# Performance work log

Measured on AMD Instinct MI355X. Metric: run time of the kernel, lower is better.

The kernel has to match this reference:

```python
import jax, jax.numpy as jnp
import numpy as np

N = 100000
E = 1000000
IN_C = 256
HID = 64
OUT = 64
NEG_SLOPE = 0.2


def setup_inputs() -> dict:
    key = jax.random.key(0)
    ks = jax.random.split(key, 12)
    x = jax.random.normal(ks[0], (N, IN_C), dtype=jnp.float32)
    edge_index = jax.random.randint(ks[1], (2, E), 0, N, dtype=jnp.int64)
    s = 1.0 / np.sqrt(IN_C)
    W1 = jax.random.uniform(ks[2], (IN_C, HID), jnp.float32, -s, s)
    a1_src = jax.random.uniform(ks[3], (HID,), jnp.float32, -s, s)
    a1_dst = jax.random.uniform(ks[4], (HID,), jnp.float32, -s, s)
    b1 = jnp.zeros((HID,), jnp.float32)
    s2 = 1.0 / np.sqrt(HID)
    W2 = jax.random.uniform(ks[5], (HID, OUT), jnp.float32, -s2, s2)
    a2_src = jax.random.uniform(ks[6], (OUT,), jnp.float32, -s2, s2)
    a2_dst = jax.random.uniform(ks[7], (OUT,), jnp.float32, -s2, s2)
    b2 = jnp.zeros((OUT,), jnp.float32)
    return {"x": x, "edge_index": edge_index, "W1": W1, "a1_src": a1_src,
            "a1_dst": a1_dst, "b1": b1, "W2": W2, "a2_src": a2_src,
            "a2_dst": a2_dst, "b2": b2}


def gat_conv(x, W, a_src, a_dst, b, src, dst):
    h = x @ W                              # [N, d]
    alpha_s = h @ a_src                    # [N]
    alpha_d = h @ a_dst                    # [N]
    e = jax.nn.leaky_relu(alpha_s[src] + alpha_d[dst], NEG_SLOPE)  # [E]
    # segment softmax over incoming edges of each destination node
    e_max = jax.lax.stop_gradient(jax.ops.segment_max(e, dst, num_segments=N))
    ex = jnp.exp(e - e_max[dst])
    denom = jax.ops.segment_sum(ex, dst, num_segments=N)
    alpha = ex / (denom[dst] + 1e-16)      # [E]
    out = jax.ops.segment_sum(alpha[:, None] * h[src], dst, num_segments=N)
    return out + b


def reference(x, edge_index, W1, a1_src, a1_dst, b1, W2, a2_src, a2_dst, b2):
    src, dst = edge_index[0], edge_index[1]
    # dropout(p=0.6) is identity in eval mode
    h = jax.nn.relu(gat_conv(x, W1, a1_src, a1_dst, b1, src, dst))
    out = gat_conv(h, W2, a2_src, a2_dst, b2, src, dst)
    return out
```

## Files before the change

### kernel.cpp

```cpp
#include <hip/hip_runtime.h>
#include <math.h>

#define HID 64
#define BSH 9
#define NPB 512
#define EPB 4096
#define CAP 8192

typedef __attribute__((ext_vector_type(8))) short bf16x8;
typedef __attribute__((ext_vector_type(4))) float f32x4;
typedef __attribute__((ext_vector_type(4))) unsigned int u32x4;
typedef __attribute__((ext_vector_type(2))) unsigned int u32x2;

__device__ __forceinline__ unsigned short f2bf(float f) {
    unsigned u = __float_as_uint(f);
    unsigned r = u + 0x7FFF + ((u >> 16) & 1);
    return (unsigned short)(r >> 16);
}


__global__ __launch_bounds__(256) void prep_kernel(const float* __restrict__ W1,
                                                   const float* __restrict__ W2,
                                                   unsigned short* __restrict__ Wt1,
                                                   unsigned short* __restrict__ Wt2,
                                                   int* __restrict__ bcnt) {
    int t = threadIdx.x, blk = blockIdx.x;
    int n = t & 63;
    if (blk == 0) bcnt[t] = 0;
    if (blk < 64) {
        int k = blk * 4 + (t >> 6);
        Wt1[(size_t)n * 256 + k] = f2bf(W1[(size_t)k * 64 + n]);
    } else {
        int k = (blk - 64) * 4 + (t >> 6);
        Wt2[(size_t)n * 64 + k] = f2bf(W2[(size_t)k * 64 + n]);
    }
}


__global__ __launch_bounds__(256) void scatter_gemm1(
    const int* __restrict__ esrc, const int* __restrict__ edst,
    int* __restrict__ bcnt, int* __restrict__ ebuf, int E_, int NB, int SB,
    const float* __restrict__ Xf, const unsigned short* __restrict__ Wt,
    const float* __restrict__ a_s, const float* __restrict__ a_d,
    unsigned short* __restrict__ C, float* __restrict__ as_,
    float* __restrict__ ad_, int Nrows) {
    constexpr int K = 256, KPAD = K + 8, XPAD = 72;
    __shared__ union {
        unsigned short gemm[64 * KPAD + 128 * XPAD];
        struct { int hist[256]; int chunk[256]; int lcur[256]; } sc;
    } sh;
    int t = threadIdx.x;

    if ((int)blockIdx.x < SB) {
        sh.sc.hist[t] = 0;
        sh.sc.lcur[t] = 0;
        __syncthreads();
        int base = blockIdx.x * EPB;
        int lim = E_ - base;
        if (lim > EPB) lim = EPB;
        for (int i = t; i < lim; i += 256) {
            atomicAdd(&sh.sc.hist[edst[base + i] >> BSH], 1);
        }
        __syncthreads();
        if (t < NB) sh.sc.chunk[t] = sh.sc.hist[t] ? atomicAdd(&bcnt[t], sh.sc.hist[t]) : 0;
        __syncthreads();
        for (int i = t; i < lim; i += 256) {
            int sv = esrc[base + i];
            int dv = edst[base + i];
            int b = dv >> BSH;
            int pos = sh.sc.chunk[b] + atomicAdd(&sh.sc.lcur[b], 1);
            ebuf[b * CAP + pos] = (sv << BSH) | (dv & (NPB - 1));
        }
        return;
    }

    unsigned short* Ws = sh.gemm;
    unsigned short* Xs = sh.gemm + 64 * KPAD;
    int n0 = ((int)blockIdx.x - SB) * 128;
    int lane = t & 63;
    int w = t >> 6;
    int m = lane & 15;
    int q = lane >> 4;
    int base = n0 + w * 32;

    constexpr int KC8 = K / 8;
    for (int i = t; i < 64 * KC8; i += 256) {
        int n = i / KC8;
        int kc = i % KC8;
        u32x4 v = *(const u32x4*)(Wt + (size_t)n * K + kc * 8);
        *(u32x4*)(&Ws[n * KPAD + kc * 8]) = v;
    }

    f32x4 acc[2][4];
#pragma unroll
    for (int mi = 0; mi < 2; ++mi)
#pragma unroll
        for (int ct = 0; ct < 4; ++ct) acc[mi][ct] = (f32x4){0.f, 0.f, 0.f, 0.f};

    for (int k0 = 0; k0 < K; k0 += 64) {
#pragma unroll
        for (int i = 0; i < 8; ++i) {
            int idx = i * 256 + t;
            int row = idx >> 4;
            int kq = (idx & 15) * 4;
            int gn = n0 + row;
            if (gn >= Nrows) gn = Nrows - 1;
            float4 v = *(const float4*)(Xf + (size_t)gn * K + k0 + kq);
            ushort4 bb;
            bb.x = f2bf(v.x); bb.y = f2bf(v.y); bb.z = f2bf(v.z); bb.w = f2bf(v.w);
            *(ushort4*)(&Xs[row * XPAD + kq]) = bb;
        }
        __syncthreads();
#pragma unroll
        for (int ks = 0; ks < 64; ks += 32) {
            bf16x8 a0 = *(const bf16x8*)(&Xs[(w * 32 + m) * XPAD + ks + q * 8]);
            bf16x8 a1 = *(const bf16x8*)(&Xs[(w * 32 + 16 + m) * XPAD + ks + q * 8]);
#pragma unroll
            for (int ct = 0; ct < 4; ++ct) {
                bf16x8 bv = *(const bf16x8*)(&Ws[(ct * 16 + m) * KPAD + k0 + ks + q * 8]);
                acc[0][ct] = __builtin_amdgcn_mfma_f32_16x16x32_bf16(a0, bv, acc[0][ct], 0, 0, 0);
                acc[1][ct] = __builtin_amdgcn_mfma_f32_16x16x32_bf16(a1, bv, acc[1][ct], 0, 0, 0);
            }
        }
        __syncthreads();
    }

    float sa0 = a_s[m], sa1 = a_s[16 + m], sa2 = a_s[32 + m], sa3 = a_s[48 + m];
    float da0 = a_d[m], da1 = a_d[16 + m], da2 = a_d[32 + m], da3 = a_d[48 + m];

#pragma unroll
    for (int mi = 0; mi < 2; ++mi) {
#pragma unroll
        for (int r = 0; r < 4; ++r) {
            int row = base + mi * 16 + q * 4 + r;
            if (row < Nrows) {
                size_t ro = (size_t)row * 64 + m;
                C[ro]      = f2bf(acc[mi][0][r]);
                C[ro + 16] = f2bf(acc[mi][1][r]);
                C[ro + 32] = f2bf(acc[mi][2][r]);
                C[ro + 48] = f2bf(acc[mi][3][r]);
            }
        }
        float vs[4], vd[4];
#pragma unroll
        for (int r = 0; r < 4; ++r) {
            float s = acc[mi][0][r] * sa0 + acc[mi][1][r] * sa1 +
                      acc[mi][2][r] * sa2 + acc[mi][3][r] * sa3;
            float d = acc[mi][0][r] * da0 + acc[mi][1][r] * da1 +
                      acc[mi][2][r] * da2 + acc[mi][3][r] * da3;
#pragma unroll
            for (int o = 1; o < 16; o <<= 1) {
                s += __shfl_xor(s, o);
                d += __shfl_xor(d, o);
            }
            vs[r] = s;
            vd[r] = d;
        }
        if (m < 4) {
            int row = base + mi * 16 + q * 4 + m;
            float wvs = (m == 0) ? vs[0] : (m == 1) ? vs[1] : (m == 2) ? vs[2] : vs[3];
            float wvd = (m == 0) ? vd[0] : (m == 1) ? vd[1] : (m == 2) ? vd[2] : vd[3];
            if (row < Nrows) {
                as_[row] = wvs;
                ad_[row] = wvd;
            }
        }
    }
}


__global__ __launch_bounds__(256) void csr_build(const int* __restrict__ ebuf,
                                                 const int* __restrict__ bcnt,
                                                 int2* __restrict__ offs,
                                                 int* __restrict__ srcs, int Nv) {
    __shared__ int dhist[NPB], dbase[NPB], psum[256];
    int b = blockIdx.x, t = threadIdx.x;
    int cnt = bcnt[b];
    int e0 = b * CAP;
#pragma unroll
    for (int j = t; j < NPB; j += 256) dhist[j] = 0;
    __syncthreads();
    for (int i = t; i < cnt; i += 256) {
        atomicAdd(&dhist[ebuf[e0 + i] & (NPB - 1)], 1);
    }
    __syncthreads();
    int a0 = dhist[2 * t], a1 = dhist[2 * t + 1];
    psum[t] = a0 + a1;
    __syncthreads();
    for (int o = 1; o < 256; o <<= 1) {
        int u = (t >= o) ? psum[t - o] : 0;
        __syncthreads();
        psum[t] += u;
        __syncthreads();
    }
    int ex = psum[t] - (a0 + a1);
    dbase[2 * t] = ex;
    dbase[2 * t + 1] = ex + a0;
    __syncthreads();
#pragma unroll
    for (int j = t; j < NPB; j += 256) {
        int node = (b << BSH) + j;
        if (node < Nv) {
            int beg = e0 + dbase[j];
            offs[node] = make_int2(beg, beg + dhist[j]);
        }
    }
    __syncthreads();
    for (int i = t; i < cnt; i += 256) {
        int e = ebuf[e0 + i];
        int pos = atomicAdd(&dbase[e & (NPB - 1)], 1);
        srcs[e0 + pos] = e >> BSH;
    }
}


template <int K, bool BF16IN>
__global__ __launch_bounds__(256) void gemm_mfma(const void* __restrict__ Xv,
                                                 const unsigned short* __restrict__ Wt,
                                                 const float* __restrict__ a_s,
                                                 const float* __restrict__ a_d,
                                                 unsigned short* __restrict__ C,
                                                 float* __restrict__ as_,
                                                 float* __restrict__ ad_, int Nrows) {
    constexpr int KPAD = K + 8;
    constexpr int XPAD = 72;
    __shared__ __align__(16) unsigned short Ws[64 * KPAD];
    __shared__ __align__(16) unsigned short Xs[128 * XPAD];

    const float* Xf = (const float*)Xv;
    const unsigned short* Xb = (const unsigned short*)Xv;

    int t = threadIdx.x;
    int n0 = blockIdx.x * 128;
    int lane = t & 63;
    int w = t >> 6;
    int m = lane & 15;
    int q = lane >> 4;
    int base = n0 + w * 32;

    constexpr int KC8 = K / 8;
    for (int i = t; i < 64 * KC8; i += 256) {
        int n = i / KC8;
        int kc = i % KC8;
        u32x4 v = *(const u32x4*)(Wt + (size_t)n * K + kc * 8);
        *(u32x4*)(&Ws[n * KPAD + kc * 8]) = v;
    }

    f32x4 acc[2][4];
#pragma unroll
    for (int mi = 0; mi < 2; ++mi)
#pragma unroll
        for (int ct = 0; ct < 4; ++ct) acc[mi][ct] = (f32x4){0.f, 0.f, 0.f, 0.f};

    for (int k0 = 0; k0 < K; k0 += 64) {
        if (!BF16IN) {
#pragma unroll
            for (int i = 0; i < 8; ++i) {
                int idx = i * 256 + t;
                int row = idx >> 4;
                int kq = (idx & 15) * 4;
                int gn = n0 + row;
                if (gn >= Nrows) gn = Nrows - 1;
                float4 v = *(const float4*)(Xf + (size_t)gn * K + k0 + kq);
                ushort4 bb;
                bb.x = f2bf(v.x); bb.y = f2bf(v.y); bb.z = f2bf(v.z); bb.w = f2bf(v.w);
                *(ushort4*)(&Xs[row * XPAD + kq]) = bb;
            }
        } else {
#pragma unroll
            for (int i = 0; i < 4; ++i) {
                int idx = i * 256 + t;
                int row = idx >> 3;
                int kq = (idx & 7) * 8;
                int gn = n0 + row;
                if (gn >= Nrows) gn = Nrows - 1;
                u32x4 v = *(const u32x4*)(Xb + (size_t)gn * K + k0 + kq);
                *(u32x4*)(&Xs[row * XPAD + kq]) = v;
            }
        }
        __syncthreads();
#pragma unroll
        for (int ks = 0; ks < 64; ks += 32) {
            bf16x8 a0 = *(const bf16x8*)(&Xs[(w * 32 + m) * XPAD + ks + q * 8]);
            bf16x8 a1 = *(const bf16x8*)(&Xs[(w * 32 + 16 + m) * XPAD + ks + q * 8]);
#pragma unroll
            for (int ct = 0; ct < 4; ++ct) {
                bf16x8 bv = *(const bf16x8*)(&Ws[(ct * 16 + m) * KPAD + k0 + ks + q * 8]);
                acc[0][ct] = __builtin_amdgcn_mfma_f32_16x16x32_bf16(a0, bv, acc[0][ct], 0, 0, 0);
                acc[1][ct] = __builtin_amdgcn_mfma_f32_16x16x32_bf16(a1, bv, acc[1][ct], 0, 0, 0);
            }
        }
        __syncthreads();
    }

    float sa0 = a_s[m], sa1 = a_s[16 + m], sa2 = a_s[32 + m], sa3 = a_s[48 + m];
    float da0 = a_d[m], da1 = a_d[16 + m], da2 = a_d[32 + m], da3 = a_d[48 + m];

#pragma unroll
    for (int mi = 0; mi < 2; ++mi) {
#pragma unroll
        for (int r = 0; r < 4; ++r) {
            int row = base + mi * 16 + q * 4 + r;
            if (row < Nrows) {
                size_t ro = (size_t)row * 64 + m;
                C[ro]      = f2bf(acc[mi][0][r]);
                C[ro + 16] = f2bf(acc[mi][1][r]);
                C[ro + 32] = f2bf(acc[mi][2][r]);
                C[ro + 48] = f2bf(acc[mi][3][r]);
            }
        }
        float vs[4], vd[4];
#pragma unroll
        for (int r = 0; r < 4; ++r) {
            float s = acc[mi][0][r] * sa0 + acc[mi][1][r] * sa1 +
                      acc[mi][2][r] * sa2 + acc[mi][3][r] * sa3;
            float d = acc[mi][0][r] * da0 + acc[mi][1][r] * da1 +
                      acc[mi][2][r] * da2 + acc[mi][3][r] * da3;
#pragma unroll
            for (int o = 1; o < 16; o <<= 1) {
                s += __shfl_xor(s, o);
                d += __shfl_xor(d, o);
            }
            vs[r] = s;
            vd[r] = d;
        }
        if (m < 4) {
            int row = base + mi * 16 + q * 4 + m;
            float wvs = (m == 0) ? vs[0] : (m == 1) ? vs[1] : (m == 2) ? vs[2] : vs[3];
            float wvd = (m == 0) ? vd[0] : (m == 1) ? vd[1] : (m == 2) ? vd[2] : vd[3];
            if (row < Nrows) {
                as_[row] = wvs;
                ad_[row] = wvd;
            }
        }
    }
}


#define GATHER_CHUNK(sC, pC, BASE_E)                                          \
    {                                                                         \
        int rem = cnt - (BASE_E);                                             \
        if (rem > 0) {                                                        \
            int nb = rem < 16 ? ((rem + 7) & ~7) : 16;                        \
            for (int j = 0; j < nb; j += 8) {                                 \
                u32x2 hv[8];                                                  \
                float pv[8];                                                  \
                _Pragma("unroll") for (int u = 0; u < 8; ++u) {               \
                    int idx = qsel | (j + u);                                 \
                    int su = __shfl(sC, idx);                                 \
                    pv[u] = __shfl(pC, idx);                                  \
                    hv[u] = *(const u32x2*)(Hp + (size_t)su * HID);           \
                }                                                             \
                _Pragma("unroll") for (int u = 0; u < 8; ++u) {               \
                    acc0 += pv[u] * __uint_as_float(hv[u].x << 16);           \
                    acc1 += pv[u] * __uint_as_float(hv[u].x & 0xFFFF0000u);   \
                    acc2 += pv[u] * __uint_as_float(hv[u].y << 16);           \
                    acc3 += pv[u] * __uint_as_float(hv[u].y & 0xFFFF0000u);   \
                }                                                             \
            }                                                                 \
        }                                                                     \
    }

template <bool RELU_BF16OUT>
__global__ __launch_bounds__(256) void agg_kernel(const unsigned short* __restrict__ H,
                                                  const float* __restrict__ as_,
                                                  const float* __restrict__ ad_,
                                                  const float* __restrict__ bias,
                                                  const int2* __restrict__ offs,
                                                  const int* __restrict__ srcs,
                                                  void* __restrict__ outp, int Nrows) {
    int t = threadIdx.x;
    int lane = t & 63;
    int q16 = lane & 15;
    int qsel = lane & 48;
    int d = blockIdx.x * 16 + ((t >> 6) << 2) + (qsel >> 4);
    if (d >= Nrows) return;
    int2 oe = offs[d];
    int begin = oe.x;
    int cnt = oe.y - oe.x;
    if (cnt > 64) cnt = 64;
    float adv = ad_[d];

    int s0 = 0, s1 = 0, s2 = 0, s3 = 0;
    float p0 = 0.f, p1 = 0.f, p2 = 0.f, p3 = 0.f;
    if (q16 < cnt) {
        s0 = srcs[begin + q16];
        float xv = as_[s0] + adv;
        xv = (xv > 0.f) ? xv : 0.2f * xv;
        p0 = __expf(xv);
    }
    if (16 + q16 < cnt) {
        s1 = srcs[begin + 16 + q16];
        float xv = as_[s1] + adv;
        xv = (xv > 0.f) ? xv : 0.2f * xv;
        p1 = __expf(xv);
    }
    if (32 + q16 < cnt) {
        s2 = srcs[begin + 32 + q16];
        float xv = as_[s2] + adv;
        xv = (xv > 0.f) ? xv : 0.2f * xv;
        p2 = __expf(xv);
    }
    if (48 + q16 < cnt) {
        s3 = srcs[begin + 48 + q16];
        float xv = as_[s3] + adv;
        xv = (xv > 0.f) ? xv : 0.2f * xv;
        p3 = __expf(xv);
    }
    float lsum = (p0 + p1) + (p2 + p3);
#pragma unroll
    for (int o = 1; o < 16; o <<= 1) lsum += __shfl_xor(lsum, o);

    float acc0 = 0.f, acc1 = 0.f, acc2 = 0.f, acc3 = 0.f;
    const unsigned short* Hp = H + 4 * q16;
    GATHER_CHUNK(s0, p0, 0)
    GATHER_CHUNK(s1, p1, 16)
    GATHER_CHUNK(s2, p2, 32)
    GATHER_CHUNK(s3, p3, 48)

    float inv = 1.f / (lsum + 1e-16f);
    float4 bv = *(const float4*)(bias + 4 * q16);
    float o0 = acc0 * inv + bv.x;
    float o1 = acc1 * inv + bv.y;
    float o2 = acc2 * inv + bv.z;
    float o3 = acc3 * inv + bv.w;
    if (RELU_BF16OUT) {
        u32x2 pkd;
        pkd.x = ((unsigned)f2bf(fmaxf(o1, 0.f)) << 16) | f2bf(fmaxf(o0, 0.f));
        pkd.y = ((unsigned)f2bf(fmaxf(o3, 0.f)) << 16) | f2bf(fmaxf(o2, 0.f));
        *(u32x2*)((unsigned short*)outp + (size_t)d * HID + 4 * q16) = pkd;
    } else {
        *(float4*)((float*)outp + (size_t)d * HID + 4 * q16) =
            make_float4(o0, o1, o2, o3);
    }
}


extern "C" void kernel_launch(void* const* d_in, const int* in_sizes, int n_in,
                              void* d_out, int out_size, void* d_ws, size_t ws_size,
                              hipStream_t stream) {
    const float* x      = (const float*)d_in[0];
    const int*   edge   = (const int*)d_in[1];
    const float* W1     = (const float*)d_in[2];
    const float* a1_src = (const float*)d_in[3];
    const float* a1_dst = (const float*)d_in[4];
    const float* b1     = (const float*)d_in[5];
    const float* W2     = (const float*)d_in[6];
    const float* a2_src = (const float*)d_in[7];
    const float* a2_dst = (const float*)d_in[8];
    const float* b2     = (const float*)d_in[9];
    float* out = (float*)d_out;

    const int N = in_sizes[0] / 256;
    const int E = in_sizes[1] / 2;
    const int IN_C = 256;
    const int NB = (N + NPB - 1) >> BSH;

    char* w = (char*)d_ws;
    auto alloc = [&](size_t bytes) {
        char* p = w;
        w += (bytes + 255) & ~(size_t)255;
        return p;
    };
    int2*           offs = (int2*)alloc((size_t)N * 8);
    int*            srcs = (int*)alloc((size_t)NB * CAP * 4);
    int*            ebuf = (int*)alloc((size_t)NB * CAP * 4);
    int*            bcnt = (int*)alloc(256 * 4);
    unsigned short* h1   = (unsigned short*)alloc((size_t)N * HID * 2);
    unsigned short* hB   = (unsigned short*)alloc((size_t)N * HID * 2);
    float*          as_  = (float*)alloc((size_t)N * 4);
    float*          ad_  = (float*)alloc((size_t)N * 4);
    unsigned short* Wt1  = (unsigned short*)alloc((size_t)IN_C * 64 * 2);
    unsigned short* Wt2  = (unsigned short*)alloc((size_t)64 * 64 * 2);

    const int* esrc = edge;
    const int* edst = edge + E;

    prep_kernel<<<IN_C / 4 + 64 / 4, 256, 0, stream>>>(W1, W2, Wt1, Wt2, bcnt);

    int SB = (E + EPB - 1) / EPB;
    int gblocks = (N + 127) / 128;
    scatter_gemm1<<<SB + gblocks, 256, 0, stream>>>(esrc, edst, bcnt, ebuf, E, NB, SB,
                                                    x, Wt1, a1_src, a1_dst, h1, as_, ad_, N);
    csr_build<<<NB, 256, 0, stream>>>(ebuf, bcnt, offs, srcs, N);

    int ablocks = (N + 15) / 16;
    agg_kernel<true><<<ablocks, 256, 0, stream>>>(h1, as_, ad_, b1, offs, srcs, hB, N);

    gemm_mfma<64, true><<<gblocks, 256, 0, stream>>>(hB, Wt2, a2_src, a2_dst, h1, as_, ad_, N);
    agg_kernel<false><<<ablocks, 256, 0, stream>>>(h1, as_, ad_, b2, offs, srcs, out, N);
}
```

Measured before the change: 269.2 us.

## Split scatter from GEMM1 and load GEMM1 operands directly into registers

The fused scatter+GEMM1 launch is split back into separate bucket_scatter, csr_build and gemm1_kernel launches. GEMM1 no longer stages W and X through LDS: each lane loads its X row fragments and W column fragments from global memory straight into MFMA operand registers. This drops LDS traffic and barriers and lets the kernel declare 4 blocks per CU, at the cost of losing the overlap between scatter and GEMM and re-reading W from L2 in every wave.

Result: slower. 286.7 us (+6.5%).

```diff
diff --git a/kernel.cpp b/kernel.cpp
--- a/kernel.cpp
+++ b/kernel.cpp
@@ -37,59 +37,103 @@
 }
 
 
-__global__ __launch_bounds__(256) void scatter_gemm1(
-    const int* __restrict__ esrc, const int* __restrict__ edst,
-    int* __restrict__ bcnt, int* __restrict__ ebuf, int E_, int NB, int SB,
+__global__ __launch_bounds__(256) void bucket_scatter(const int* __restrict__ esrc,
+                                                      const int* __restrict__ edst,
+                                                      int* __restrict__ bcnt,
+                                                      int* __restrict__ ebuf, int E_, int NB) {
+    __shared__ int hist[256], chunk[256], lcur[256];
+    int t = threadIdx.x;
+    hist[t] = 0;
+    lcur[t] = 0;
+    __syncthreads();
+    int base = blockIdx.x * EPB;
+    int lim = E_ - base;
+    if (lim > EPB) lim = EPB;
+    for (int i = t; i < lim; i += 256) {
+        atomicAdd(&hist[edst[base + i] >> BSH], 1);
+    }
+    __syncthreads();
+    if (t < NB) chunk[t] = hist[t] ? atomicAdd(&bcnt[t], hist[t]) : 0;
+    __syncthreads();
+    for (int i = t; i < lim; i += 256) {
+        int sv = esrc[base + i];
+        int dv = edst[base + i];
+        int b = dv >> BSH;
+        int pos = chunk[b] + atomicAdd(&lcur[b], 1);
+        ebuf[b * CAP + pos] = (sv << BSH) | (dv & (NPB - 1));
+    }
+}
+
+
+__global__ __launch_bounds__(256) void csr_build(const int* __restrict__ ebuf,
+                                                 const int* __restrict__ bcnt,
+                                                 int2* __restrict__ offs,
+                                                 int* __restrict__ srcs, int Nv) {
+    __shared__ int dhist[NPB], dbase[NPB], psum[256];
+    int b = blockIdx.x, t = threadIdx.x;
+    int cnt = bcnt[b];
+    int e0 = b * CAP;
+#pragma unroll
+    for (int j = t; j < NPB; j += 256) dhist[j] = 0;
+    __syncthreads();
+    for (int i = t; i < cnt; i += 256) {
+        atomicAdd(&dhist[ebuf[e0 + i] & (NPB - 1)], 1);
+    }
+    __syncthreads();
+    int a0 = dhist[2 * t], a1 = dhist[2 * t + 1];
+    psum[t] = a0 + a1;
+    __syncthreads();
+    for (int o = 1; o < 256; o <<= 1) {
+        int u = (t >= o) ? psum[t - o] : 0;
+        __syncthreads();
+        psum[t] += u;
+        __syncthreads();
+    }
+    int ex = psum[t] - (a0 + a1);
+    dbase[2 * t] = ex;
+    dbase[2 * t + 1] = ex + a0;
+    __syncthreads();
+#pragma unroll
+    for (int j = t; j < NPB; j += 256) {
+        int node = (b << BSH) + j;
+        if (node < Nv) {
+            int beg = e0 + dbase[j];
+            offs[node] = make_int2(beg, beg + dhist[j]);
+        }
+    }
+    __syncthreads();
+    for (int i = t; i < cnt; i += 256) {
+        int e = ebuf[e0 + i];
+        int pos = atomicAdd(&dbase[e & (NPB - 1)], 1);
+        srcs[e0 + pos] = e >> BSH;
+    }
+}
+
+
+__global__ __launch_bounds__(256, 4) void gemm1_kernel(
     const float* __restrict__ Xf, const unsigned short* __restrict__ Wt,
     const float* __restrict__ a_s, const float* __restrict__ a_d,
     unsigned short* __restrict__ C, float* __restrict__ as_,
     float* __restrict__ ad_, int Nrows) {
-    constexpr int K = 256, KPAD = K + 8, XPAD = 72;
-    __shared__ union {
-        unsigned short gemm[64 * KPAD + 128 * XPAD];
-        struct { int hist[256]; int chunk[256]; int lcur[256]; } sc;
-    } sh;
+    constexpr int K = 256;
     int t = threadIdx.x;
-
-    if ((int)blockIdx.x < SB) {
-        sh.sc.hist[t] = 0;
-        sh.sc.lcur[t] = 0;
-        __syncthreads();
-        int base = blockIdx.x * EPB;
-        int lim = E_ - base;
-        if (lim > EPB) lim = EPB;
-        for (int i = t; i < lim; i += 256) {
-            atomicAdd(&sh.sc.hist[edst[base + i] >> BSH], 1);
-        }
-        __syncthreads();
-        if (t < NB) sh.sc.chunk[t] = sh.sc.hist[t] ? atomicAdd(&bcnt[t], sh.sc.hist[t]) : 0;
-        __syncthreads();
-        for (int i = t; i < lim; i += 256) {
-            int sv = esrc[base + i];
-            int dv = edst[base + i];
-            int b = dv >> BSH;
-            int pos = sh.sc.chunk[b] + atomicAdd(&sh.sc.lcur[b], 1);
-            ebuf[b * CAP + pos] = (sv << BSH) | (dv & (NPB - 1));
-        }
-        return;
-    }
-
-    unsigned short* Ws = sh.gemm;
-    unsigned short* Xs = sh.gemm + 64 * KPAD;
-    int n0 = ((int)blockIdx.x - SB) * 128;
+    int n0 = blockIdx.x * 128;
     int lane = t & 63;
     int w = t >> 6;
     int m = lane & 15;
     int q = lane >> 4;
     int base = n0 + w * 32;
-
-    constexpr int KC8 = K / 8;
-    for (int i = t; i < 64 * KC8; i += 256) {
-        int n = i / KC8;
-        int kc = i % KC8;
-        u32x4 v = *(const u32x4*)(Wt + (size_t)n * K + kc * 8);
-        *(u32x4*)(&Ws[n * KPAD + kc * 8]) = v;
-    }
+    int gn0 = base + m;
+    int gn1 = base + 16 + m;
+    if (gn0 >= Nrows) gn0 = Nrows - 1;
+    if (gn1 >= Nrows) gn1 = Nrows - 1;
+
+    const float* xr0 = Xf + (size_t)gn0 * K;
+    const float* xr1 = Xf + (size_t)gn1 * K;
+    const unsigned short* wb0 = Wt + (size_t)(0 * 16 + m) * K;
+    const unsigned short* wb1 = Wt + (size_t)(1 * 16 + m) * K;
+    const unsigned short* wb2 = Wt + (size_t)(2 * 16 + m) * K;
+    const unsigned short* wb3 = Wt + (size_t)(3 * 16 + m) * K;
 
     f32x4 acc[2][4];
 #pragma unroll
@@ -97,32 +141,34 @@
 #pragma unroll
         for (int ct = 0; ct < 4; ++ct) acc[mi][ct] = (f32x4){0.f, 0.f, 0.f, 0.f};
 
-    for (int k0 = 0; k0 < K; k0 += 64) {
-#pragma unroll
-        for (int i = 0; i < 8; ++i) {
-            int idx = i * 256 + t;
-            int row = idx >> 4;
-            int kq = (idx & 15) * 4;
-            int gn = n0 + row;
-            if (gn >= Nrows) gn = Nrows - 1;
-            float4 v = *(const float4*)(Xf + (size_t)gn * K + k0 + kq);
-            ushort4 bb;
-            bb.x = f2bf(v.x); bb.y = f2bf(v.y); bb.z = f2bf(v.z); bb.w = f2bf(v.w);
-            *(ushort4*)(&Xs[row * XPAD + kq]) = bb;
-        }
-        __syncthreads();
-#pragma unroll
-        for (int ks = 0; ks < 64; ks += 32) {
-            bf16x8 a0 = *(const bf16x8*)(&Xs[(w * 32 + m) * XPAD + ks + q * 8]);
-            bf16x8 a1 = *(const bf16x8*)(&Xs[(w * 32 + 16 + m) * XPAD + ks + q * 8]);
-#pragma unroll
-            for (int ct = 0; ct < 4; ++ct) {
-                bf16x8 bv = *(const bf16x8*)(&Ws[(ct * 16 + m) * KPAD + k0 + ks + q * 8]);
-                acc[0][ct] = __builtin_amdgcn_mfma_f32_16x16x32_bf16(a0, bv, acc[0][ct], 0, 0, 0);
-                acc[1][ct] = __builtin_amdgcn_mfma_f32_16x16x32_bf16(a1, bv, acc[1][ct], 0, 0, 0);
-            }
-        }
-        __syncthreads();
+#pragma unroll
+    for (int kk = 0; kk < K; kk += 32) {
+        int col = kk + q * 8;
+        float4 v0 = *(const float4*)(xr0 + col);
+        float4 v1 = *(const float4*)(xr0 + col + 4);
+        float4 v2 = *(const float4*)(xr1 + col);
+        float4 v3 = *(const float4*)(xr1 + col + 4);
+        bf16x8 b0 = *(const bf16x8*)(wb0 + col);
+        bf16x8 b1 = *(const bf16x8*)(wb1 + col);
+        bf16x8 b2 = *(const bf16x8*)(wb2 + col);
+        bf16x8 b3 = *(const bf16x8*)(wb3 + col);
+        bf16x8 a0, a1;
+        a0[0] = (short)f2bf(v0.x); a0[1] = (short)f2bf(v0.y);
+        a0[2] = (short)f2bf(v0.z); a0[3] = (short)f2bf(v0.w);
+        a0[4] = (short)f2bf(v1.x); a0[5] = (short)f2bf(v1.y);
+        a0[6] = (short)f2bf(v1.z); a0[7] = (short)f2bf(v1.w);
+        a1[0] = (short)f2bf(v2.x); a1[1] = (short)f2bf(v2.y);
+        a1[2] = (short)f2bf(v2.z); a1[3] = (short)f2bf(v2.w);
+        a1[4] = (short)f2bf(v3.x); a1[5] = (short)f2bf(v3.y);
+        a1[6] = (short)f2bf(v3.z); a1[7] = (short)f2bf(v3.w);
+        acc[0][0] = __builtin_amdgcn_mfma_f32_16x16x32_bf16(a0, b0, acc[0][0], 0, 0, 0);
+        acc[1][0] = __builtin_amdgcn_mfma_f32_16x16x32_bf16(a1, b0, acc[1][0], 0, 0, 0);
+        acc[0][1] = __builtin_amdgcn_mfma_f32_16x16x32_bf16(a0, b1, acc[0][1], 0, 0, 0);
+        acc[1][1] = __builtin_amdgcn_mfma_f32_16x16x32_bf16(a1, b1, acc[1][1], 0, 0, 0);
+        acc[0][2] = __builtin_amdgcn_mfma_f32_16x16x32_bf16(a0, b2, acc[0][2], 0, 0, 0);
+        acc[1][2] = __builtin_amdgcn_mfma_f32_16x16x32_bf16(a1, b2, acc[1][2], 0, 0, 0);
+        acc[0][3] = __builtin_amdgcn_mfma_f32_16x16x32_bf16(a0, b3, acc[0][3], 0, 0, 0);
+        acc[1][3] = __builtin_amdgcn_mfma_f32_16x16x32_bf16(a1, b3, acc[1][3], 0, 0, 0);
     }
 
     float sa0 = a_s[m], sa1 = a_s[16 + m], sa2 = a_s[32 + m], sa3 = a_s[48 + m];
@@ -165,51 +211,6 @@
                 ad_[row] = wvd;
             }
         }
-    }
-}
-
-
-__global__ __launch_bounds__(256) void csr_build(const int* __restrict__ ebuf,
-                                                 const int* __restrict__ bcnt,
-                                                 int2* __restrict__ offs,
-                                                 int* __restrict__ srcs, int Nv) {
-    __shared__ int dhist[NPB], dbase[NPB], psum[256];
-    int b = blockIdx.x, t = threadIdx.x;
-    int cnt = bcnt[b];
-    int e0 = b * CAP;
-#pragma unroll
-    for (int j = t; j < NPB; j += 256) dhist[j] = 0;
-    __syncthreads();
-    for (int i = t; i < cnt; i += 256) {
-        atomicAdd(&dhist[ebuf[e0 + i] & (NPB - 1)], 1);
-    }
-    __syncthreads();
-    int a0 = dhist[2 * t], a1 = dhist[2 * t + 1];
-    psum[t] = a0 + a1;
-    __syncthreads();
-    for (int o = 1; o < 256; o <<= 1) {
-        int u = (t >= o) ? psum[t - o] : 0;
-        __syncthreads();
-        psum[t] += u;
-        __syncthreads();
-    }
-    int ex = psum[t] - (a0 + a1);
-    dbase[2 * t] = ex;
-    dbase[2 * t + 1] = ex + a0;
-    __syncthreads();
-#pragma unroll
-    for (int j = t; j < NPB; j += 256) {
-        int node = (b << BSH) + j;
-        if (node < Nv) {
-            int beg = e0 + dbase[j];
-            offs[node] = make_int2(beg, beg + dhist[j]);
-        }
-    }
-    __syncthreads();
-    for (int i = t; i < cnt; i += 256) {
-        int e = ebuf[e0 + i];
-        int pos = atomicAdd(&dbase[e & (NPB - 1)], 1);
-        srcs[e0 + pos] = e >> BSH;
     }
 }
 
@@ -478,13 +479,14 @@
 
     prep_kernel<<<IN_C / 4 + 64 / 4, 256, 0, stream>>>(W1, W2, Wt1, Wt2, bcnt);
 
-    int SB = (E + EPB - 1) / EPB;
+    int gbk = (E + EPB - 1) / EPB;
+    bucket_scatter<<<gbk, 256, 0, stream>>>(esrc, edst, bcnt, ebuf, E, NB);
+    csr_build<<<NB, 256, 0, stream>>>(ebuf, bcnt, offs, srcs, N);
+
     int gblocks = (N + 127) / 128;
-    scatter_gemm1<<<SB + gblocks, 256, 0, stream>>>(esrc, edst, bcnt, ebuf, E, NB, SB,
-                                                    x, Wt1, a1_src, a1_dst, h1, as_, ad_, N);
-    csr_build<<<NB, 256, 0, stream>>>(ebuf, bcnt, offs, srcs, N);
-
     int ablocks = (N + 15) / 16;
+
+    gemm1_kernel<<<gblocks, 256, 0, stream>>>(x, Wt1, a1_src, a1_dst, h1, as_, ad_, N);
     agg_kernel<true><<<ablocks, 256, 0, stream>>>(h1, as_, ad_, b1, offs, srcs, hB, N);
 
     gemm_mfma<64, true><<<gblocks, 256, 0, stream>>>(hB, Wt2, a2_src, a2_dst, h1, as_, ad_, N);
```

## Load GEMM1 A-operand directly from global into registers with double buffering

Applied to the files above, without the earlier changes.

The first-layer GEMM no longer stages X tiles through shared memory. Each lane loads its own fp32 row slices straight into registers, converts them to bf16 in registers, and feeds them to MFMA. Two register buffers let loads for the next half-row overlap with compute on the current one. This removes the LDS round trip and the per-k-chunk barriers, and it shrinks LDS use, which may raise occupancy. The costs are higher register pressure and a less coalesced global access pattern, since each lane reads 32-byte pieces of different rows.

After: 272.8 us. No clear change (+1.3%).

```diff
diff --git a/kernel.cpp b/kernel.cpp
--- a/kernel.cpp
+++ b/kernel.cpp
@@ -44,9 +44,9 @@
     const float* __restrict__ a_s, const float* __restrict__ a_d,
     unsigned short* __restrict__ C, float* __restrict__ as_,
     float* __restrict__ ad_, int Nrows) {
-    constexpr int K = 256, KPAD = K + 8, XPAD = 72;
+    constexpr int K = 256, KPAD = K + 8;
     __shared__ union {
-        unsigned short gemm[64 * KPAD + 128 * XPAD];
+        unsigned short ws[64 * KPAD];
         struct { int hist[256]; int chunk[256]; int lcur[256]; } sc;
     } sh;
     int t = threadIdx.x;
@@ -74,8 +74,7 @@
         return;
     }
 
-    unsigned short* Ws = sh.gemm;
-    unsigned short* Xs = sh.gemm + 64 * KPAD;
+    unsigned short* Ws = sh.ws;
     int n0 = ((int)blockIdx.x - SB) * 128;
     int lane = t & 63;
     int w = t >> 6;
@@ -90,6 +89,15 @@
         u32x4 v = *(const u32x4*)(Wt + (size_t)n * K + kc * 8);
         *(u32x4*)(&Ws[n * KPAD + kc * 8]) = v;
     }
+    __syncthreads();
+
+    int gn0 = base + m;
+    int gn1 = base + 16 + m;
+    if (gn0 >= Nrows) gn0 = Nrows - 1;
+    if (gn1 >= Nrows) gn1 = Nrows - 1;
+    const float* xr0 = Xf + (size_t)gn0 * K;
+    const float* xr1 = Xf + (size_t)gn1 * K;
+    int colq = q * 8;
 
     f32x4 acc[2][4];
 #pragma unroll
@@ -97,33 +105,50 @@
 #pragma unroll
         for (int ct = 0; ct < 4; ++ct) acc[mi][ct] = (f32x4){0.f, 0.f, 0.f, 0.f};
 
-    for (int k0 = 0; k0 < K; k0 += 64) {
-#pragma unroll
-        for (int i = 0; i < 8; ++i) {
-            int idx = i * 256 + t;
-            int row = idx >> 4;
-            int kq = (idx & 15) * 4;
-            int gn = n0 + row;
-            if (gn >= Nrows) gn = Nrows - 1;
-            float4 v = *(const float4*)(Xf + (size_t)gn * K + k0 + kq);
-            ushort4 bb;
-            bb.x = f2bf(v.x); bb.y = f2bf(v.y); bb.z = f2bf(v.z); bb.w = f2bf(v.w);
-            *(ushort4*)(&Xs[row * XPAD + kq]) = bb;
-        }
-        __syncthreads();
-#pragma unroll
-        for (int ks = 0; ks < 64; ks += 32) {
-            bf16x8 a0 = *(const bf16x8*)(&Xs[(w * 32 + m) * XPAD + ks + q * 8]);
-            bf16x8 a1 = *(const bf16x8*)(&Xs[(w * 32 + 16 + m) * XPAD + ks + q * 8]);
-#pragma unroll
-            for (int ct = 0; ct < 4; ++ct) {
-                bf16x8 bv = *(const bf16x8*)(&Ws[(ct * 16 + m) * KPAD + k0 + ks + q * 8]);
-                acc[0][ct] = __builtin_amdgcn_mfma_f32_16x16x32_bf16(a0, bv, acc[0][ct], 0, 0, 0);
-                acc[1][ct] = __builtin_amdgcn_mfma_f32_16x16x32_bf16(a1, bv, acc[1][ct], 0, 0, 0);
-            }
-        }
-        __syncthreads();
-    }
+    float4 buf0[8], buf1[8];
+
+#pragma unroll
+    for (int i = 0; i < 4; ++i) {
+        buf0[2 * i]     = *(const float4*)(xr0 + i * 32 + colq);
+        buf0[2 * i + 1] = *(const float4*)(xr0 + i * 32 + colq + 4);
+    }
+#pragma unroll
+    for (int i = 0; i < 4; ++i) {
+        buf1[2 * i]     = *(const float4*)(xr0 + 128 + i * 32 + colq);
+        buf1[2 * i + 1] = *(const float4*)(xr0 + 128 + i * 32 + colq + 4);
+    }
+
+#define CONSUME(BUF, MI, KBASE)                                               \
+    _Pragma("unroll") for (int i = 0; i < 4; ++i) {                           \
+        float4 v0 = BUF[2 * i], v1 = BUF[2 * i + 1];                          \
+        bf16x8 a;                                                             \
+        a[0] = (short)f2bf(v0.x); a[1] = (short)f2bf(v0.y);                   \
+        a[2] = (short)f2bf(v0.z); a[3] = (short)f2bf(v0.w);                   \
+        a[4] = (short)f2bf(v1.x); a[5] = (short)f2bf(v1.y);                   \
+        a[6] = (short)f2bf(v1.z); a[7] = (short)f2bf(v1.w);                   \
+        int kc = (KBASE) + i * 32 + colq;                                     \
+        _Pragma("unroll") for (int ct = 0; ct < 4; ++ct) {                    \
+            bf16x8 bv = *(const bf16x8*)(&Ws[(ct * 16 + m) * KPAD + kc]);     \
+            acc[MI][ct] =                                                     \
+                __builtin_amdgcn_mfma_f32_16x16x32_bf16(a, bv, acc[MI][ct], 0, 0, 0); \
+        }                                                                     \
+    }
+
+    CONSUME(buf0, 0, 0)
+#pragma unroll
+    for (int i = 0; i < 4; ++i) {
+        buf0[2 * i]     = *(const float4*)(xr1 + i * 32 + colq);
+        buf0[2 * i + 1] = *(const float4*)(xr1 + i * 32 + colq + 4);
+    }
+    CONSUME(buf1, 0, 128)
+#pragma unroll
+    for (int i = 0; i < 4; ++i) {
+        buf1[2 * i]     = *(const float4*)(xr1 + 128 + i * 32 + colq);
+        buf1[2 * i + 1] = *(const float4*)(xr1 + 128 + i * 32 + colq + 4);
+    }
+    CONSUME(buf0, 1, 0)
+    CONSUME(buf1, 1, 128)
+#undef CONSUME
 
     float sa0 = a_s[m], sa1 = a_s[16 + m], sa2 = a_s[32 + m], sa3 = a_s[48 + m];
     float da0 = a_d[m], da1 = a_d[16 + m], da2 = a_d[32 + m], da3 = a_d[48 + m];
```
